# Kernel tuning notes

Hardware: AMD Instinct MI355X
Metric: run time of the kernel (lower is better)

## Reference

```python
import jax, jax.numpy as jnp
import numpy as np

D = 1024
H = 16
HD = D // H
B = 4
L = 2048
FFN = 4 * D
EPS = 1e-5


def _layer_norm(x, g, b):
    mu = jnp.mean(x, axis=-1, keepdims=True)
    var = jnp.mean(jnp.square(x - mu), axis=-1, keepdims=True)
    return (x - mu) * jax.lax.rsqrt(var + EPS) * g + b


def setup_inputs() -> dict:
    key = jax.random.key(0)
    ks = jax.random.split(key, 16)
    s = 1.0 / np.sqrt(D)
    inp = {
        "x": jax.random.normal(ks[0], (B, L, D), dtype=jnp.float32),
        "rel_pos_bias": jax.random.normal(ks[1], (1, H, L, L), dtype=jnp.float32) * 0.02,
        "wq": jax.random.normal(ks[2], (D, D), dtype=jnp.float32) * s,
        "bq": jnp.zeros((D,), jnp.float32),
        "wk": jax.random.normal(ks[3], (D, D), dtype=jnp.float32) * s,
        "bk": jnp.zeros((D,), jnp.float32),
        "wv": jax.random.normal(ks[4], (D, D), dtype=jnp.float32) * s,
        "bv": jnp.zeros((D,), jnp.float32),
        "wo": jax.random.normal(ks[5], (D, D), dtype=jnp.float32) * s,
        "bo": jnp.zeros((D,), jnp.float32),
        "g1": jnp.ones((D,), jnp.float32),
        "be1": jnp.zeros((D,), jnp.float32),
        "g2": jnp.ones((D,), jnp.float32),
        "be2": jnp.zeros((D,), jnp.float32),
        "w1": jax.random.normal(ks[6], (D, FFN), dtype=jnp.float32) * s,
        "bf1": jnp.zeros((FFN,), jnp.float32),
        "w2": jax.random.normal(ks[7], (FFN, D), dtype=jnp.float32) * (1.0 / np.sqrt(FFN)),
        "bf2": jnp.zeros((D,), jnp.float32),
    }
    return inp


def reference(x, rel_pos_bias, wq, bq, wk, bk, wv, bv, wo, bo,
              g1, be1, g2, be2, w1, bf1, w2, bf2):
    scale = HD ** -0.5
    residual = x
    xn = _layer_norm(x, g1, be1)
    # projections -> (B, H, L, HD)
    q = (xn @ wq + bq).reshape(B, L, H, HD).transpose(0, 2, 1, 3)
    k = (xn @ wk + bk).reshape(B, L, H, HD).transpose(0, 2, 1, 3)
    v = (xn @ wv + bv).reshape(B, L, H, HD).transpose(0, 2, 1, 3)
    scores = jnp.einsum('bhqd,bhkd->bhqk', q, k) * scale
    causal = jnp.tril(jnp.ones((L, L), dtype=bool))
    scores = jnp.where(causal[None, None], scores, -jnp.inf)
    scores = scores + rel_pos_bias
    attn = jax.nn.softmax(scores, axis=-1)
    out = jnp.einsum('bhqk,bhkd->bhqd', attn, v)
    out = out.transpose(0, 2, 1, 3).reshape(B, L, D)
    out = out @ wo + bo
    x = residual + out
    residual = x
    xn = _layer_norm(x, g2, be2)
    h = jax.nn.relu(xn @ w1 + bf1)
    x = residual + (h @ w2 + bf2)
    return x
```

## Files before the change

kernel.cpp:

```cpp
#include <hip/hip_runtime.h>
#include <hip/hip_bf16.h>

#define D_   1024
#define H_   16
#define HD_  64
#define B_   4
#define L_   2048
#define FFN_ 4096
#define M_   (B_ * L_)

typedef __bf16 bf16x8 __attribute__((ext_vector_type(8)));
typedef float f32x4 __attribute__((ext_vector_type(4)));
typedef unsigned short ushort8 __attribute__((ext_vector_type(8)));
typedef unsigned short ushort4v __attribute__((ext_vector_type(4)));

__device__ inline unsigned short f2bf(float f) {
    unsigned int u = __float_as_uint(f);
    u += 0x7fff + ((u >> 16) & 1);
    return (unsigned short)(u >> 16);
}

__device__ inline void gl_lds16(const unsigned short* g, unsigned short* l) {
    __builtin_amdgcn_global_load_lds(
        (const __attribute__((address_space(1))) unsigned int*)g,
        (__attribute__((address_space(3))) unsigned int*)l, 16, 0, 0);
}

__global__ __launch_bounds__(256) void k_transpose_bf16(
    const float* __restrict__ in, unsigned short* __restrict__ out, int K, int N)
{
    __shared__ float tile[64][65];
    int k0 = blockIdx.y * 64, n0 = blockIdx.x * 64;
    int t = threadIdx.x;
    int r = t >> 2, cs = (t & 3) * 16;
    const float* src = in + (size_t)(k0 + r) * N + n0 + cs;
#pragma unroll
    for (int i = 0; i < 16; i += 4) {
        float4 v = *(const float4*)(src + i);
        tile[r][cs + i + 0] = v.x;
        tile[r][cs + i + 1] = v.y;
        tile[r][cs + i + 2] = v.z;
        tile[r][cs + i + 3] = v.w;
    }
    __syncthreads();
    unsigned short* dst = out + (size_t)(n0 + r) * K + k0 + cs;
#pragma unroll
    for (int i = 0; i < 16; ++i) dst[i] = f2bf(tile[cs + i][r]);
}

__global__ void k_concat_bias(const float* __restrict__ bq, const float* __restrict__ bk,
                              const float* __restrict__ bv, float* __restrict__ out)
{
    int i = blockIdx.x * 256 + threadIdx.x;
    float v = (i < 1024) ? bq[i] : (i < 2048 ? bk[i - 1024] : bv[i - 2048]);
    out[i] = v;
}

__global__ __launch_bounds__(256) void k_layernorm(
    const float* __restrict__ x, const float* __restrict__ g, const float* __restrict__ be,
    unsigned short* __restrict__ out)
{
    int row = blockIdx.x;
    const float* xr = x + (size_t)row * D_;
    int t = threadIdx.x;
    float4 v = *(const float4*)(xr + t * 4);
    float s = v.x + v.y + v.z + v.w;
    float sq = v.x * v.x + v.y * v.y + v.z * v.z + v.w * v.w;
#pragma unroll
    for (int off = 32; off >= 1; off >>= 1) {
        s  += __shfl_down(s, off);
        sq += __shfl_down(sq, off);
    }
    __shared__ float ps[4], psq[4];
    int w = t >> 6;
    if ((t & 63) == 0) { ps[w] = s; psq[w] = sq; }
    __syncthreads();
    float tot  = ps[0] + ps[1] + ps[2] + ps[3];
    float totq = psq[0] + psq[1] + psq[2] + psq[3];
    float mu  = tot * (1.f / D_);
    float var = totq * (1.f / D_) - mu * mu;
    float inv = rsqrtf(var + 1e-5f);
    float4 gv = *(const float4*)(g + t * 4);
    float4 bv = *(const float4*)(be + t * 4);
    ushort4v o;
    o[0] = f2bf((v.x - mu) * inv * gv.x + bv.x);
    o[1] = f2bf((v.y - mu) * inv * gv.y + bv.y);
    o[2] = f2bf((v.z - mu) * inv * gv.z + bv.z);
    o[3] = f2bf((v.w - mu) * inv * gv.w + bv.w);
    *(ushort4v*)(out + (size_t)row * D_ + t * 4) = o;
}

template <int BM, int BN, int WM, int WN, bool OUT_BF16, bool RELU, bool RESID>
__global__ __launch_bounds__(WM * WN * 64, 2) void k_gemm4(
    const unsigned short* __restrict__ A, const unsigned short* __restrict__ Bt,
    const float* __restrict__ bias, const float* __restrict__ resid,
    void* __restrict__ Cout, int M, int N, int K)
{
    constexpr int NW  = WM * WN;
    constexpr int MS  = BM / WM;
    constexpr int NS  = BN / WN;
    constexpr int MI  = MS / 16;
    constexpr int NI  = NS / 16;
    constexpr int APW = BM / (8 * NW);
    constexpr int BPW = BN / (8 * NW);

    __shared__ unsigned short sA[2][BM * 64];
    __shared__ unsigned short sB[2][BN * 64];

    int nwg = gridDim.x, flat = blockIdx.x;
    int wg = (flat & 7) * (nwg >> 3) + (flat >> 3);
    int gx = N / BN;
    int m0 = (wg / gx) * BM, n0 = (wg % gx) * BN;

    int tid = threadIdx.x, lane = tid & 63, wv = tid >> 6;
    int wr = wv / WN, wc = wv % WN;
    int wm = wr * MS, wn = wc * NS;
    int lr = lane & 15, qd = lane >> 4;

    f32x4 acc[MI][NI] = {};

    int r8 = lane >> 3, c8 = lane & 7;
    int csw = ((c8 ^ (r8 & 7)) * 8);
    const unsigned short* gA[APW];
    const unsigned short* gB[BPW];
    int laA[APW], laB[BPW];
#pragma unroll
    for (int s = 0; s < APW; ++s) {
        int rl = wv * 8 * APW + s * 8;
        gA[s]  = A + (size_t)(m0 + rl + r8) * K + csw;
        laA[s] = rl * 64;
    }
#pragma unroll
    for (int s = 0; s < BPW; ++s) {
        int rl = wv * 8 * BPW + s * 8;
        gB[s]  = Bt + (size_t)(n0 + rl + r8) * K + csw;
        laB[s] = rl * 64;
    }

#pragma unroll
    for (int s = 0; s < APW; ++s) gl_lds16(gA[s], &sA[0][laA[s]]);
#pragma unroll
    for (int s = 0; s < BPW; ++s) gl_lds16(gB[s], &sB[0][laB[s]]);

    int nk = K >> 6;
    for (int ki = 0; ki < nk; ++ki) {
        int cur = ki & 1;
        __syncthreads();
        if (ki + 1 < nk) {
            int k1 = (ki + 1) << 6;
#pragma unroll
            for (int s = 0; s < APW; ++s) gl_lds16(gA[s] + k1, &sA[cur ^ 1][laA[s]]);
#pragma unroll
            for (int s = 0; s < BPW; ++s) gl_lds16(gB[s] + k1, &sB[cur ^ 1][laB[s]]);
        }
#pragma unroll
        for (int ks = 0; ks < 2; ++ks) {
            bf16x8 af[MI], bfr[NI];
#pragma unroll
            for (int i = 0; i < MI; ++i) {
                int row = wm + i * 16 + lr;
                int p = ((ks * 4 + qd) ^ (lr & 7)) * 8;
                af[i] = *(const bf16x8*)(&sA[cur][row * 64 + p]);
            }
#pragma unroll
            for (int i = 0; i < NI; ++i) {
                int row = wn + i * 16 + lr;
                int p = ((ks * 4 + qd) ^ (lr & 7)) * 8;
                bfr[i] = *(const bf16x8*)(&sB[cur][row * 64 + p]);
            }
            __builtin_amdgcn_s_setprio(1);
#pragma unroll
            for (int mi = 0; mi < MI; ++mi)
#pragma unroll
                for (int ni = 0; ni < NI; ++ni)
                    acc[mi][ni] = __builtin_amdgcn_mfma_f32_16x16x32_bf16(
                        bfr[ni], af[mi], acc[mi][ni], 0, 0, 0);
            __builtin_amdgcn_s_setprio(0);
        }
    }

#pragma unroll
    for (int mi = 0; mi < MI; ++mi) {
        int row = m0 + wm + mi * 16 + lr;
#pragma unroll
        for (int ni = 0; ni < NI; ++ni) {
            int col = n0 + wn + ni * 16 + qd * 4;
            float4 bv4 = *(const float4*)(bias + col);
            f32x4 a = acc[mi][ni];
            float4 o;
            o.x = a[0] + bv4.x; o.y = a[1] + bv4.y;
            o.z = a[2] + bv4.z; o.w = a[3] + bv4.w;
            if (RELU) {
                o.x = fmaxf(o.x, 0.f); o.y = fmaxf(o.y, 0.f);
                o.z = fmaxf(o.z, 0.f); o.w = fmaxf(o.w, 0.f);
            }
            if (RESID) {
                float4 rr = *(const float4*)(resid + (size_t)row * N + col);
                o.x += rr.x; o.y += rr.y; o.z += rr.z; o.w += rr.w;
            }
            if (OUT_BF16) {
                ushort4v u;
                u[0] = f2bf(o.x); u[1] = f2bf(o.y);
                u[2] = f2bf(o.z); u[3] = f2bf(o.w);
                *(ushort4v*)((unsigned short*)Cout + (size_t)row * N + col) = u;
            } else {
                *(float4*)((float*)Cout + (size_t)row * N + col) = o;
            }
        }
    }
}

__global__ __launch_bounds__(256, 4) void k_attn(
    const unsigned short* __restrict__ qkv, const float* __restrict__ rpb,
    unsigned short* __restrict__ out)
{
    __shared__ unsigned short Ks[64 * 72];
    __shared__ unsigned short Vt[64 * 64];
    __shared__ unsigned short Sp[64 * 72];

    int flat = blockIdx.x;
    int xcd = flat & 7, b = (flat >> 3) & 3, hi = flat >> 5;
    int g = hi * 8 + xcd;
    int h = g & 15;
    int qt = 31 - (g >> 4);
    int q0 = qt * 64;

    int t = threadIdx.x, lane = t & 63, w = t >> 6;
    int lr = lane & 15, qd = lane >> 4;
    int sr = t >> 2, ss = (t & 3) * 16;
    int bL = b * L_;

    bf16x8 aq[2];
    {
        const unsigned short* qsrc =
            qkv + (size_t)(bL + q0 + w * 16 + lr) * 3072 + h * 64 + qd * 8;
        aq[0] = *(const bf16x8*)qsrc;
        aq[1] = *(const bf16x8*)(qsrc + 32);
    }

    f32x4 oacc[4] = {};
    float m_r[4], l_r[4];
#pragma unroll
    for (int r = 0; r < 4; ++r) { m_r[r] = -1e30f; l_r[r] = 0.f; }

    int qrow_base = q0 + w * 16 + qd * 4;
    int ntile = qt + 1;

    ushort8 krA, krB, vrA, vrB;
    {
        const unsigned short* kb_ = qkv + (size_t)(bL + sr) * 3072 + 1024 + h * 64 + ss;
        krA = *(const ushort8*)kb_;  krB = *(const ushort8*)(kb_ + 8);
        vrA = *(const ushort8*)(kb_ + 1024); vrB = *(const ushort8*)(kb_ + 1032);
    }

    for (int kt = 0; kt < ntile; ++kt) {
        int k0 = kt * 64;
        if (kt) __syncthreads();

        *(ushort8*)(Ks + sr * 72 + ss)     = krA;
        *(ushort8*)(Ks + sr * 72 + ss + 8) = krB;

        {
            int role = sr & 1;
            int srp  = sr & ~1;
#pragma unroll
            for (int i = 0; i < 8; ++i) {
                int sendv = role ? (int)(unsigned int)vrA[i] : (int)(unsigned int)vrB[i];
                int got = __shfl_xor(sendv, 4);
                int d = role ? (ss + 8 + i) : (ss + i);
                unsigned short lo = role ? (unsigned short)got : vrA[i];
                unsigned short hi = role ? vrB[i] : (unsigned short)got;
                int swz = (d ^ (d >> 3)) & 7;
                unsigned int u = (unsigned int)lo | ((unsigned int)hi << 16);
                *(unsigned int*)(Vt + d * 64 + (srp ^ (swz << 3))) = u;
            }
        }
        __syncthreads();

        float rv[4][4];
        {
            const float* rpb_base = rpb + ((size_t)h * L_ + qrow_base) * L_ + k0;
#pragma unroll
            for (int r = 0; r < 4; ++r)
#pragma unroll
                for (int nt = 0; nt < 4; ++nt)
                    rv[r][nt] = rpb_base[(size_t)r * L_ + nt * 16 + lr];
        }

        if (kt + 1 < ntile) {
            const unsigned short* kb_ =
                qkv + (size_t)(bL + k0 + 64 + sr) * 3072 + 1024 + h * 64 + ss;
            krA = *(const ushort8*)kb_;  krB = *(const ushort8*)(kb_ + 8);
            vrA = *(const ushort8*)(kb_ + 1024); vrB = *(const ushort8*)(kb_ + 1032);
        }

        f32x4 sc4[4] = {};
        __builtin_amdgcn_s_setprio(1);
#pragma unroll
        for (int ks = 0; ks < 2; ++ks) {
#pragma unroll
            for (int nt = 0; nt < 4; ++nt) {
                bf16x8 bk8 = *(const bf16x8*)(Ks + (nt * 16 + lr) * 72 + ks * 32 + qd * 8);
                sc4[nt] = __builtin_amdgcn_mfma_f32_16x16x32_bf16(aq[ks], bk8, sc4[nt], 0, 0, 0);
            }
        }
        __builtin_amdgcn_s_setprio(0);

        bool last = (kt == qt);
        float pvv[4][4], mx[4];
#pragma unroll
        for (int r = 0; r < 4; ++r) {
            mx[r] = -1e30f;
#pragma unroll
            for (int nt = 0; nt < 4; ++nt) {
                float sv = sc4[nt][r] * 0.125f + rv[r][nt];
                if (last && (k0 + nt * 16 + lr > qrow_base + r)) sv = -1e30f;
                pvv[r][nt] = sv;
                mx[r] = fmaxf(mx[r], sv);
            }
        }
#pragma unroll
        for (int r = 0; r < 4; ++r) {
            mx[r] = fmaxf(mx[r], __shfl_xor(mx[r], 1));
            mx[r] = fmaxf(mx[r], __shfl_xor(mx[r], 2));
            mx[r] = fmaxf(mx[r], __shfl_xor(mx[r], 4));
            mx[r] = fmaxf(mx[r], __shfl_xor(mx[r], 8));
        }
#pragma unroll
        for (int r = 0; r < 4; ++r) {
            float mnew  = fmaxf(m_r[r], mx[r]);
            float alpha = __expf(m_r[r] - mnew);
            float psum = 0.f;
#pragma unroll
            for (int nt = 0; nt < 4; ++nt) {
                float p = __expf(pvv[r][nt] - mnew);
                psum += p;
                Sp[(w * 16 + qd * 4 + r) * 72 + nt * 16 + lr] = f2bf(p);
            }
            psum += __shfl_xor(psum, 1);
            psum += __shfl_xor(psum, 2);
            psum += __shfl_xor(psum, 4);
            psum += __shfl_xor(psum, 8);
            l_r[r] = l_r[r] * alpha + psum;
            m_r[r] = mnew;
            oacc[0][r] *= alpha; oacc[1][r] *= alpha;
            oacc[2][r] *= alpha; oacc[3][r] *= alpha;
        }

        __builtin_amdgcn_s_setprio(1);
#pragma unroll
        for (int ks = 0; ks < 2; ++ks) {
            bf16x8 ap = *(const bf16x8*)(Sp + (w * 16 + lr) * 72 + ks * 32 + qd * 8);
#pragma unroll
            for (int dt = 0; dt < 4; ++dt) {
                int d = dt * 16 + lr;
                int swz = (d ^ (d >> 3)) & 7;
                bf16x8 bv8 = *(const bf16x8*)(Vt + d * 64 + ((ks * 32 + qd * 8) ^ (swz << 3)));
                oacc[dt] = __builtin_amdgcn_mfma_f32_16x16x32_bf16(ap, bv8, oacc[dt], 0, 0, 0);
            }
        }
        __builtin_amdgcn_s_setprio(0);
    }

#pragma unroll
    for (int r = 0; r < 4; ++r) {
        float linv = 1.f / l_r[r];
        int qrow = q0 + w * 16 + qd * 4 + r;
        unsigned short* dst = out + (size_t)(bL + qrow) * 1024 + h * 64;
#pragma unroll
        for (int dt = 0; dt < 4; ++dt)
            dst[dt * 16 + lr] = f2bf(oacc[dt][r] * linv);
    }
}

extern "C" void kernel_launch(void* const* d_in, const int* in_sizes, int n_in,
                              void* d_out, int out_size, void* d_ws, size_t ws_size,
                              hipStream_t stream)
{
    const float* x   = (const float*)d_in[0];
    const float* rpb = (const float*)d_in[1];
    const float* wq  = (const float*)d_in[2];
    const float* bq  = (const float*)d_in[3];
    const float* wk  = (const float*)d_in[4];
    const float* bk  = (const float*)d_in[5];
    const float* wv  = (const float*)d_in[6];
    const float* bv  = (const float*)d_in[7];
    const float* wo  = (const float*)d_in[8];
    const float* bo  = (const float*)d_in[9];
    const float* g1  = (const float*)d_in[10];
    const float* be1 = (const float*)d_in[11];
    const float* g2  = (const float*)d_in[12];
    const float* be2 = (const float*)d_in[13];
    const float* w1  = (const float*)d_in[14];
    const float* bf1 = (const float*)d_in[15];
    const float* w2  = (const float*)d_in[16];
    const float* bf2 = (const float*)d_in[17];
    float* out = (float*)d_out;
    char* ws = (char*)d_ws;

    unsigned short* xn1   = (unsigned short*)(ws + 0);
    unsigned short* qkv   = (unsigned short*)(ws + 16777216);
    unsigned short* attno = (unsigned short*)(ws + 0);
    unsigned short* hbuf  = (unsigned short*)(ws + 0);
    float*          xmid  = (float*)(ws + 67108864);
    unsigned short* xn2   = (unsigned short*)(ws + 100663296);
    unsigned short* wqkvT = (unsigned short*)(ws + 117440512);
    unsigned short* woT   = (unsigned short*)(ws + 123731968);
    unsigned short* w1T   = (unsigned short*)(ws + 125829120);
    unsigned short* w2T   = (unsigned short*)(ws + 134217728);
    float*          bqkv  = (float*)(ws + 142606336);

    k_transpose_bf16<<<dim3(16, 16), 256, 0, stream>>>(wq, wqkvT,                1024, 1024);
    k_transpose_bf16<<<dim3(16, 16), 256, 0, stream>>>(wk, wqkvT + 1024 * 1024,  1024, 1024);
    k_transpose_bf16<<<dim3(16, 16), 256, 0, stream>>>(wv, wqkvT + 2048 * 1024,  1024, 1024);
    k_transpose_bf16<<<dim3(16, 16), 256, 0, stream>>>(wo, woT,                  1024, 1024);
    k_transpose_bf16<<<dim3(64, 16), 256, 0, stream>>>(w1, w1T,                  1024, 4096);
    k_transpose_bf16<<<dim3(16, 64), 256, 0, stream>>>(w2, w2T,                  4096, 1024);
    k_concat_bias<<<12, 256, 0, stream>>>(bq, bk, bv, bqkv);

    k_layernorm<<<M_, 256, 0, stream>>>(x, g1, be1, xn1);
    k_gemm4<256, 256, 2, 4, true, false, false><<<dim3(384), 512, 0, stream>>>(
        xn1, wqkvT, bqkv, nullptr, qkv, M_, 3072, 1024);
    k_attn<<<dim3(2048), 256, 0, stream>>>(qkv, rpb, attno);
    k_gemm4<256, 128, 4, 2, false, false, true><<<dim3(256), 512, 0, stream>>>(
        attno, woT, bo, x, xmid, M_, 1024, 1024);
    k_layernorm<<<M_, 256, 0, stream>>>(xmid, g2, be2, xn2);
    k_gemm4<256, 256, 2, 4, true, true, false><<<dim3(512), 512, 0, stream>>>(
        xn2, w1T, bf1, nullptr, hbuf, M_, 4096, 1024);
    k_gemm4<256, 128, 4, 2, false, false, true><<<dim3(256), 512, 0, stream>>>(
        hbuf, w2T, bf2, xmid, out, M_, 1024, 4096);
}
```

Measured before the change: 856.0 us.

## Switch GEMMs to triple-buffered LDS pipeline with fixed 256x128 tiles

Replaces the templated double-buffered GEMM with a fixed 256x128-tile kernel that keeps two K-slices in flight using three LDS buffers. Explicit vmcnt waits plus a raw s_barrier replace __syncthreads, so global-to-LDS loads overlap more with MFMA work. The QKV and FFN1 GEMMs move from 256x256 to 256x128 tiles, which doubles their block count and reduces per-block reuse. LDS use grows to 144KB per block, which may limit occupancy to one block per CU despite the launch bounds.

```diff
diff --git a/kernel.cpp b/kernel.cpp
--- a/kernel.cpp
+++ b/kernel.cpp
@@ -90,69 +90,76 @@
     *(ushort4v*)(out + (size_t)row * D_ + t * 4) = o;
 }
 
-template <int BM, int BN, int WM, int WN, bool OUT_BF16, bool RELU, bool RESID>
-__global__ __launch_bounds__(WM * WN * 64, 2) void k_gemm4(
+template <bool OUT_BF16, bool RELU, bool RESID>
+__global__ __launch_bounds__(512, 2) void k_gemm5(
     const unsigned short* __restrict__ A, const unsigned short* __restrict__ Bt,
     const float* __restrict__ bias, const float* __restrict__ resid,
     void* __restrict__ Cout, int M, int N, int K)
 {
-    constexpr int NW  = WM * WN;
-    constexpr int MS  = BM / WM;
-    constexpr int NS  = BN / WN;
-    constexpr int MI  = MS / 16;
-    constexpr int NI  = NS / 16;
-    constexpr int APW = BM / (8 * NW);
-    constexpr int BPW = BN / (8 * NW);
-
-    __shared__ unsigned short sA[2][BM * 64];
-    __shared__ unsigned short sB[2][BN * 64];
+    constexpr int BM = 256, BN = 128;
+    constexpr int MI = 4, NI = 4;
+    __shared__ unsigned short sA[3][BM * 64];
+    __shared__ unsigned short sB[3][BN * 64];
 
     int nwg = gridDim.x, flat = blockIdx.x;
     int wg = (flat & 7) * (nwg >> 3) + (flat >> 3);
-    int gx = N / BN;
+    int gx = N >> 7;
     int m0 = (wg / gx) * BM, n0 = (wg % gx) * BN;
 
     int tid = threadIdx.x, lane = tid & 63, wv = tid >> 6;
-    int wr = wv / WN, wc = wv % WN;
-    int wm = wr * MS, wn = wc * NS;
+    int wr = wv >> 1, wc = wv & 1;
+    int wm = wr * 64, wn = wc * 64;
     int lr = lane & 15, qd = lane >> 4;
 
     f32x4 acc[MI][NI] = {};
 
     int r8 = lane >> 3, c8 = lane & 7;
-    int csw = ((c8 ^ (r8 & 7)) * 8);
-    const unsigned short* gA[APW];
-    const unsigned short* gB[BPW];
-    int laA[APW], laB[BPW];
-#pragma unroll
-    for (int s = 0; s < APW; ++s) {
-        int rl = wv * 8 * APW + s * 8;
+    int csw = (c8 ^ (r8 & 7)) * 8;
+    const unsigned short* gA[4]; const unsigned short* gB[2];
+    int laA[4], laB[2];
+#pragma unroll
+    for (int s = 0; s < 4; ++s) {
+        int rl = wv * 32 + s * 8;
         gA[s]  = A + (size_t)(m0 + rl + r8) * K + csw;
         laA[s] = rl * 64;
     }
 #pragma unroll
-    for (int s = 0; s < BPW; ++s) {
-        int rl = wv * 8 * BPW + s * 8;
+    for (int s = 0; s < 2; ++s) {
+        int rl = wv * 16 + s * 8;
         gB[s]  = Bt + (size_t)(n0 + rl + r8) * K + csw;
         laB[s] = rl * 64;
     }
 
-#pragma unroll
-    for (int s = 0; s < APW; ++s) gl_lds16(gA[s], &sA[0][laA[s]]);
-#pragma unroll
-    for (int s = 0; s < BPW; ++s) gl_lds16(gB[s], &sB[0][laB[s]]);
-
     int nk = K >> 6;
-    for (int ki = 0; ki < nk; ++ki) {
-        int cur = ki & 1;
-        __syncthreads();
-        if (ki + 1 < nk) {
-            int k1 = (ki + 1) << 6;
-#pragma unroll
-            for (int s = 0; s < APW; ++s) gl_lds16(gA[s] + k1, &sA[cur ^ 1][laA[s]]);
-#pragma unroll
-            for (int s = 0; s < BPW; ++s) gl_lds16(gB[s] + k1, &sB[cur ^ 1][laB[s]]);
-        }
+#pragma unroll
+    for (int s = 0; s < 4; ++s) gl_lds16(gA[s], &sA[0][laA[s]]);
+#pragma unroll
+    for (int s = 0; s < 2; ++s) gl_lds16(gB[s], &sB[0][laB[s]]);
+#pragma unroll
+    for (int s = 0; s < 4; ++s) gl_lds16(gA[s] + 64, &sA[1][laA[s]]);
+#pragma unroll
+    for (int s = 0; s < 2; ++s) gl_lds16(gB[s] + 64, &sB[1][laB[s]]);
+
+    int cur = 0;
+    for (int t = 0; t < nk; ++t) {
+        if (t + 1 < nk) {
+            asm volatile("s_waitcnt vmcnt(6)" ::: "memory");
+        } else {
+            asm volatile("s_waitcnt vmcnt(0)" ::: "memory");
+        }
+        __builtin_amdgcn_sched_barrier(0);
+        __builtin_amdgcn_s_barrier();
+        __builtin_amdgcn_sched_barrier(0);
+
+        if (t + 2 < nk) {
+            int k2 = (t + 2) << 6;
+            int nb = cur + 2; if (nb >= 3) nb -= 3;
+#pragma unroll
+            for (int s = 0; s < 4; ++s) gl_lds16(gA[s] + k2, &sA[nb][laA[s]]);
+#pragma unroll
+            for (int s = 0; s < 2; ++s) gl_lds16(gB[s] + k2, &sB[nb][laB[s]]);
+        }
+
 #pragma unroll
         for (int ks = 0; ks < 2; ++ks) {
             bf16x8 af[MI], bfr[NI];
@@ -177,6 +184,7 @@
                         bfr[ni], af[mi], acc[mi][ni], 0, 0, 0);
             __builtin_amdgcn_s_setprio(0);
         }
+        cur = (cur == 2) ? 0 : cur + 1;
     }
 
 #pragma unroll
@@ -419,14 +427,14 @@
     k_concat_bias<<<12, 256, 0, stream>>>(bq, bk, bv, bqkv);
 
     k_layernorm<<<M_, 256, 0, stream>>>(x, g1, be1, xn1);
-    k_gemm4<256, 256, 2, 4, true, false, false><<<dim3(384), 512, 0, stream>>>(
+    k_gemm5<true, false, false><<<dim3(768), 512, 0, stream>>>(
         xn1, wqkvT, bqkv, nullptr, qkv, M_, 3072, 1024);
     k_attn<<<dim3(2048), 256, 0, stream>>>(qkv, rpb, attno);
-    k_gemm4<256, 128, 4, 2, false, false, true><<<dim3(256), 512, 0, stream>>>(
+    k_gemm5<false, false, true><<<dim3(256), 512, 0, stream>>>(
         attno, woT, bo, x, xmid, M_, 1024, 1024);
     k_layernorm<<<M_, 256, 0, stream>>>(xmid, g2, be2, xn2);
-    k_gemm4<256, 256, 2, 4, true, true, false><<<dim3(512), 512, 0, stream>>>(
+    k_gemm5<true, true, false><<<dim3(1024), 512, 0, stream>>>(
         xn2, w1T, bf1, nullptr, hbuf, M_, 4096, 1024);
-    k_gemm4<256, 128, 4, 2, false, false, true><<<dim3(256), 512, 0, stream>>>(
+    k_gemm5<false, false, true><<<dim3(256), 512, 0, stream>>>(
         hbuf, w2T, bf2, xmid, out, M_, 1024, 4096);
 }
```

Result: slower. 886.4 us (+3.6%).
